# Kernel optimization log

Hardware: AMD Instinct MI355X
Metric: run time of the kernel (lower is better)

Reference implementation:

```python
import jax, jax.numpy as jnp
import numpy as np
from jax import lax

P = 8; E = 192; D_MODEL = E + 4; D_STATE = 16; D_CONV = 4; EXPAND = 2
D_INNER = EXPAND * D_MODEL  # 392
DT_RANK = -(-D_MODEL // 16)  # 13
MAX_FREQ = 32


def silu(v):
    return v * jax.nn.sigmoid(v)


def layernorm(v, g, b, eps=1e-5):
    m = v.mean(-1, keepdims=True)
    var = v.var(-1, keepdims=True)
    return (v - m) / jnp.sqrt(var + eps) * g + b


def mamba(x, in_w, conv_w, conv_b, xp_w, dt_w, dt_b, A_log, Dp, out_w):
    # Standard mamba_ssm Mamba block. x: (B, L, d_model)
    B, L, _ = x.shape
    xz = x @ in_w.T                      # (B,L,2*d_inner)
    xi, z = jnp.split(xz, 2, axis=-1)
    # depthwise causal conv1d (torch pads d_conv-1 both sides then truncates to L)
    xc = jnp.transpose(xi, (0, 2, 1))    # (B,d_inner,L)
    xc = lax.conv_general_dilated(xc, conv_w[:, None, :], (1,), [(D_CONV - 1, 0)],
                                  dimension_numbers=('NCH', 'OIH', 'NCH'),
                                  feature_group_count=D_INNER)
    xc = silu(jnp.transpose(xc, (0, 2, 1)) + conv_b)  # (B,L,d_inner)
    x_dbl = xc @ xp_w.T                  # (B,L,dt_rank+2*d_state)
    dt = x_dbl[..., :DT_RANK]
    Bm = x_dbl[..., DT_RANK:DT_RANK + D_STATE]
    Cm = x_dbl[..., DT_RANK + D_STATE:]
    delta = jax.nn.softplus(dt @ dt_w.T + dt_b)       # (B,L,d_inner)
    A = -jnp.exp(A_log)                               # (d_inner,d_state)
    deltaA = jnp.exp(delta[..., None] * A)            # (B,L,d_inner,d_state)
    deltaBu = delta[..., None] * Bm[:, :, None, :] * xc[..., None]

    def step(h, inp):
        dA, dBu, c = inp
        h = dA * h + dBu
        return h, jnp.einsum('bdn,bn->bd', h, c)

    h0 = jnp.zeros((B, D_INNER, D_STATE), x.dtype)
    _, ys = lax.scan(step, h0, (deltaA.transpose(1, 0, 2, 3),
                                deltaBu.transpose(1, 0, 2, 3),
                                Cm.transpose(1, 0, 2)))
    y = ys.transpose(1, 0, 2) + Dp * xc
    y = y * silu(z)
    return y @ out_w.T


def _mk_mamba_params(key):
    ks = jax.random.split(key, 6)
    s = 0.05
    return dict(
        in_w=jax.random.normal(ks[0], (2 * D_INNER, D_MODEL)) * s,
        conv_w=jax.random.normal(ks[1], (D_INNER, D_CONV)) * s,
        conv_b=jnp.zeros((D_INNER,)),
        xp_w=jax.random.normal(ks[2], (DT_RANK + 2 * D_STATE, D_INNER)) * s,
        dt_w=jax.random.normal(ks[3], (D_INNER, DT_RANK)) * s,
        dt_b=jax.random.normal(ks[4], (D_INNER,)) * 0.1,
        A_log=jnp.log(jnp.broadcast_to(jnp.arange(1, D_STATE + 1, dtype=jnp.float32), (D_INNER, D_STATE)) + 0.0),
        D=jnp.ones((D_INNER,)),
        out_w=jax.random.normal(ks[5], (D_MODEL, D_INNER)) * s,
    )


def setup_inputs() -> dict:
    key = jax.random.key(0)
    k = jax.random.split(key, 8)
    inp = {
        'x': jax.random.normal(k[0], (16, 3, 256, 256), dtype=jnp.float32),
        'patch_w': jax.random.normal(k[1], (E, 3, P, P)) * 0.05,
        'patch_b': jnp.zeros((E,)),
        'pe_ln_g': jnp.ones((E,)), 'pe_ln_b': jnp.zeros((E,)),
        'blk_ln_g': jnp.ones((D_MODEL,)), 'blk_ln_b': jnp.zeros((D_MODEL,)),
        'cls_w': jax.random.normal(k[2], (1, D_MODEL)) * 0.05,
        'cls_b': jnp.zeros((1,)),
    }
    for pref, kk in (('f_', k[3]), ('b_', k[4])):
        for name, val in _mk_mamba_params(kk).items():
            inp[pref + name] = val
    return inp


def reference(x, patch_w, patch_b, pe_ln_g, pe_ln_b,
              f_in_w, f_conv_w, f_conv_b, f_xp_w, f_dt_w, f_dt_b, f_A_log, f_D, f_out_w,
              b_in_w, b_conv_w, b_conv_b, b_xp_w, b_dt_w, b_dt_b, b_A_log, b_D, b_out_w,
              blk_ln_g, blk_ln_b, cls_w, cls_b):
    B, C, H, W = x.shape
    hp, wp = H // P, W // P
    # PatchEmbed: stride==kernel conv expressed as one GEMM over patches
    xp = x.reshape(B, C, hp, P, wp, P)
    tok = jnp.einsum('bchpwq,ecpq->bhwe', xp, patch_w) + patch_b
    tok = tok.reshape(B, hp * wp, E)
    tok = silu(layernorm(tok, pe_ln_g, pe_ln_b))
    # RotaryEmbedding: concat 4 positional channels
    L = hp * wp
    scale = 2 * np.pi / MAX_FREQ
    pos = jnp.arange(L, dtype=tok.dtype)[:, None] * scale
    row = (jnp.arange(L) // MAX_FREQ).astype(tok.dtype)[:, None] * scale
    cp = jnp.concatenate([jnp.sin(pos), jnp.cos(pos), jnp.sin(row), jnp.cos(row)], axis=-1)
    h = jnp.concatenate([tok, jnp.broadcast_to(cp[None], (B, L, 4))], axis=-1)  # (B,L,196)
    # BidirectionalMambaBlock
    fo = mamba(h, f_in_w, f_conv_w, f_conv_b, f_xp_w, f_dt_w, f_dt_b, f_A_log, f_D, f_out_w)
    bo = jnp.flip(mamba(jnp.flip(h, 1), b_in_w, b_conv_w, b_conv_b, b_xp_w, b_dt_w, b_dt_b, b_A_log, b_D, b_out_w), 1)
    out = (fo + bo) * 0.5
    out = silu(layernorm(out, blk_ln_g, blk_ln_b)) + h
    # Classifier: mean pool + linear (num_classes==2 -> 1 logit)
    return out.mean(1) @ cls_w.T + cls_b
```

## Files before the change

### kernel.cpp

```cpp
#include <hip/hip_runtime.h>
#include <cstdint>
#include <cstddef>

constexpr int B_   = 16;
constexpr int L_   = 1024;
constexpr int E_   = 192;
constexpr int DM   = 196;
constexpr int DI   = 392;
constexpr int DS   = 16;
constexpr int DTR  = 13;
constexpr int NTOK = B_ * L_;
constexpr int XDW  = DTR + 2 * DS;
constexpr int CH   = B_ * DI;

constexpr int KP_XZ = 224;
constexpr int KP_OP = 416;
constexpr int KP_PW = 192;

constexpr size_t HW_SZ = (size_t)NTOK * DM;
constexpr size_t DI_SZ = (size_t)NTOK * DI;

constexpr size_t O_H     = 0;
constexpr size_t O_H16   = 3211264;
constexpr size_t O_XI_F  = 5046272;
constexpr size_t O_XI_B  = 11468800;
constexpr size_t O_Z_F   = 17891328;
constexpr size_t O_Z_B   = 24313856;
constexpr size_t O_XC_F  = 30736384;
constexpr size_t O_XC_B  = 37158912;
constexpr size_t O_DTR_F = 43581440;
constexpr size_t O_DTR_B = 43794432;
constexpr size_t O_BC_F  = 44007424;
constexpr size_t O_BC_B  = 44531712;
constexpr size_t O_YS_F  = 45056000;
constexpr size_t O_YS_B  = 48267264;
constexpr size_t O_PW16  = 51478528;
constexpr size_t O_FIN16 = 51496960;
constexpr size_t O_BIN16 = 51584768;
constexpr size_t O_FOUT16= 51672576;
constexpr size_t O_BOUT16= 51713344;

typedef _Float16 half8 __attribute__((ext_vector_type(8)));
typedef _Float16 half4v __attribute__((ext_vector_type(4)));
typedef float f32x4v __attribute__((ext_vector_type(4)));

__device__ __forceinline__ float siluf(float x) {
    return x / (1.f + __expf(-x));
}

__device__ __forceinline__ float blk_sum(float v, float* red) {
    #pragma unroll
    for (int o = 32; o > 0; o >>= 1) v += __shfl_down(v, o);
    int w = threadIdx.x >> 6;
    __syncthreads();
    if ((threadIdx.x & 63) == 0) red[w] = v;
    __syncthreads();
    return red[0] + red[1] + red[2] + red[3];
}

__global__ __launch_bounds__(256) void cvt_all(const float* __restrict__ pw,
                                               const float* __restrict__ fin,
                                               const float* __restrict__ bin,
                                               const float* __restrict__ fout,
                                               const float* __restrict__ bout,
                                               _Float16* __restrict__ dst) {
    int i = blockIdx.x * 256 + threadIdx.x;
    const float* src; int K, Kp, off;
    if (i < 36864)       { src = pw;   K = 192; Kp = 192; off = i; }
    else if (i < 212480) { src = fin;  K = 196; Kp = 224; off = i - 36864; }
    else if (i < 388096) { src = bin;  K = 196; Kp = 224; off = i - 212480; }
    else if (i < 469632) { src = fout; K = 392; Kp = 416; off = i - 388096; }
    else                 { src = bout; K = 392; Kp = 416; off = i - 469632; }
    int n = off / Kp, k = off - n * Kp;
    dst[i] = (_Float16)(k < K ? src[(size_t)n * K + k] : 0.f);
}

__global__ __launch_bounds__(256) void gather_patch(const float* __restrict__ x,
                                                    _Float16* __restrict__ Xp) {
    int i = blockIdx.x * 256 + threadIdx.x;
    int tok = i / 192, r = i - tok * 192;
    int c = r >> 6, pq = r & 63, p = pq >> 3, q = pq & 7;
    int b = tok >> 10, l = tok & 1023, hh = l >> 5, wv = l & 31;
    Xp[i] = (_Float16)x[(((size_t)(b * 3 + c) * 256 + hh * 8 + p) << 8) + wv * 8 + q];
}

template <int MODE>
__device__ __forceinline__ void mfma_core(const _Float16* __restrict__ A,
                                          const _Float16* __restrict__ W,
                                          const float* __restrict__ bias,
                                          void* __restrict__ Cv_,
                                          int N, int Kpad, int ldc,
                                          int flip, int m_blk, int n_blk) {
    const int tid = threadIdx.x;
    const int wv = tid >> 6, lane = tid & 63;
    const int col = lane & 15, quad = lane >> 4;
    const int m_base = m_blk * 128 + wv * 32;
    const int n_base = n_blk * 64;

    int r0 = m_base + col, r1 = m_base + 16 + col;
    if (flip) {
        r0 = (r0 & ~1023) + (1023 - (r0 & 1023));
        r1 = (r1 & ~1023) + (1023 - (r1 & 1023));
    }
    const _Float16* a0p = A + (size_t)r0 * Kpad + quad * 8;
    const _Float16* a1p = A + (size_t)r1 * Kpad + quad * 8;

    const _Float16* bp[4];
    bool bok[4];
    #pragma unroll
    for (int j = 0; j < 4; ++j) {
        int n = n_base + j * 16 + col;
        bok[j] = (n < N);
        bp[j] = W + (size_t)(bok[j] ? n : 0) * Kpad + quad * 8;
    }

    f32x4v acc[2][4];
    #pragma unroll
    for (int i = 0; i < 2; ++i)
        #pragma unroll
        for (int j = 0; j < 4; ++j)
            #pragma unroll
            for (int r = 0; r < 4; ++r) acc[i][j][r] = 0.f;

    half8 bzero;
    #pragma unroll
    for (int q = 0; q < 8; ++q) bzero[q] = (_Float16)0.f;

    for (int k0 = 0; k0 < Kpad; k0 += 32) {
        half8 a0 = *(const half8*)(a0p + k0);
        half8 a1 = *(const half8*)(a1p + k0);
        #pragma unroll
        for (int j = 0; j < 4; ++j) {
            half8 bv = bzero;
            if (bok[j]) bv = *(const half8*)(bp[j] + k0);
            acc[0][j] = __builtin_amdgcn_mfma_f32_16x16x32_f16(a0, bv, acc[0][j], 0, 0, 0);
            acc[1][j] = __builtin_amdgcn_mfma_f32_16x16x32_f16(a1, bv, acc[1][j], 0, 0, 0);
        }
    }

    if (MODE == 0) {
        float* C = (float*)Cv_;
        #pragma unroll
        for (int i = 0; i < 2; ++i) {
            int mrow = m_base + i * 16 + quad * 4;
            #pragma unroll
            for (int j = 0; j < 4; ++j) {
                int n = n_base + j * 16 + col;
                if (n < N) {
                    float bv = bias ? bias[n] : 0.f;
                    #pragma unroll
                    for (int r = 0; r < 4; ++r)
                        C[(size_t)(mrow + r) * ldc + n] = acc[i][j][r] + bv;
                }
            }
        }
    } else if (MODE == 4) {
        _Float16* C = (_Float16*)Cv_;
        #pragma unroll
        for (int i = 0; i < 2; ++i) {
            int mrow = m_base + i * 16 + quad * 4;
            #pragma unroll
            for (int j = 0; j < 4; ++j) {
                int n = n_base + j * 16 + col;
                if (n < N) {
                    #pragma unroll
                    for (int r = 0; r < 4; ++r)
                        C[(size_t)(mrow + r) * ldc + n] = (_Float16)acc[i][j][r];
                }
            }
        }
    } else {
        const int bb = m_base >> 10;
        const int t0 = m_base & 1023;
        #pragma unroll
        for (int i = 0; i < 2; ++i) {
            int tt = t0 + i * 16 + quad * 4;
            #pragma unroll
            for (int j = 0; j < 4; ++j) {
                int n = n_base + j * 16 + col;
                if (n < N) {
                    half4v v;
                    #pragma unroll
                    for (int r = 0; r < 4; ++r) {
                        float xx = acc[i][j][r];
                        if (MODE == 3) xx = xx / (1.f + __expf(-xx));
                        v[r] = (_Float16)xx;
                    }
                    *(half4v*)((_Float16*)Cv_ + (((size_t)(bb * N + n)) << 10) + tt) = v;
                }
            }
        }
    }
}

__global__ __launch_bounds__(256) void mfma_patch(const _Float16* __restrict__ A,
                                                  const _Float16* __restrict__ W,
                                                  const float* __restrict__ bias,
                                                  float* __restrict__ C) {
    mfma_core<0>(A, W, bias, C, 192, KP_PW, 192, 0, blockIdx.x, blockIdx.y);
}

__global__ __launch_bounds__(256) void mfma_xz(const _Float16* __restrict__ A,
                                               const _Float16* __restrict__ Wf,
                                               const _Float16* __restrict__ Wb,
                                               _Float16* __restrict__ C0, _Float16* __restrict__ C1,
                                               _Float16* __restrict__ C2, _Float16* __restrict__ C3) {
    const int zi = blockIdx.z;
    const _Float16* W = (zi < 2 ? Wf : Wb) + (size_t)(zi & 1) * DI * KP_XZ;
    const int flip = zi >> 1;
    if (zi == 0)      mfma_core<2>(A, W, nullptr, C0, DI, KP_XZ, 0, flip, blockIdx.x, blockIdx.y);
    else if (zi == 1) mfma_core<3>(A, W, nullptr, C1, DI, KP_XZ, 0, flip, blockIdx.x, blockIdx.y);
    else if (zi == 2) mfma_core<2>(A, W, nullptr, C2, DI, KP_XZ, 0, flip, blockIdx.x, blockIdx.y);
    else              mfma_core<3>(A, W, nullptr, C3, DI, KP_XZ, 0, flip, blockIdx.x, blockIdx.y);
}

__global__ __launch_bounds__(256) void mfma_op(const _Float16* __restrict__ Af,
                                               const _Float16* __restrict__ Ab,
                                               const _Float16* __restrict__ Wf,
                                               const _Float16* __restrict__ Wb,
                                               _Float16* __restrict__ Cf, _Float16* __restrict__ Cb) {
    const int zi = blockIdx.z;
    mfma_core<4>(zi ? Ab : Af, zi ? Wb : Wf, nullptr, zi ? Cb : Cf,
                 DM, KP_OP, DM, 0, blockIdx.x, blockIdx.y);
}

__global__ __launch_bounds__(256) void ln_silu_pos(const float* __restrict__ tok,
                                                   const float* __restrict__ g,
                                                   const float* __restrict__ bb,
                                                   _Float16* __restrict__ h16) {
    const int w = threadIdx.x >> 6, lane = threadIdx.x & 63;
    const int t = blockIdx.x * 4 + w;
    const float* tp = tok + (size_t)t * E_;
    float v[3];
    float s1 = 0.f, s2 = 0.f;
    #pragma unroll
    for (int i = 0; i < 3; ++i) {
        v[i] = tp[lane + i * 64];
        s1 += v[i];
        s2 = fmaf(v[i], v[i], s2);
    }
    #pragma unroll
    for (int o = 32; o > 0; o >>= 1) {
        s1 += __shfl_xor(s1, o);
        s2 += __shfl_xor(s2, o);
    }
    float mean = s1 * (1.f / E_);
    float var = s2 * (1.f / E_) - mean * mean;
    float inv = rsqrtf(var + 1e-5f);
    _Float16* hq = h16 + (size_t)t * KP_XZ;
    #pragma unroll
    for (int i = 0; i < 3; ++i) {
        int e = lane + i * 64;
        float o = siluf((v[i] - mean) * inv * g[e] + bb[e]);
        hq[e] = (_Float16)o;
    }
    const int l = t & 1023;
    const float scale = 0.19634954084936207f;
    if (lane < 4) {
        float pv = (lane == 0) ? sinf(l * scale)
                 : (lane == 1) ? cosf(l * scale)
                 : (lane == 2) ? sinf((float)(l >> 5) * scale)
                 :               cosf((float)(l >> 5) * scale);
        hq[E_ + lane] = (_Float16)pv;
    } else if (lane < 32) {
        hq[192 + lane] = (_Float16)0.f;
    }
}

__global__ __launch_bounds__(256) void gemm_xdbl(const _Float16* __restrict__ xi_f,
                                                 const _Float16* __restrict__ xi_b,
                                                 const float* __restrict__ Wf,
                                                 const float* __restrict__ Wb,
                                                 const float* __restrict__ fcw,
                                                 const float* __restrict__ fcb,
                                                 const float* __restrict__ bcw,
                                                 const float* __restrict__ bcb,
                                                 float* __restrict__ dtrf,
                                                 float* __restrict__ dtrb,
                                                 float* __restrict__ bcf,
                                                 float* __restrict__ bcb2,
                                                 float* __restrict__ xcf,
                                                 float* __restrict__ xcb) {
    const int yi = blockIdx.y;
    const _Float16* xi = yi ? xi_b : xi_f;
    const float* W = yi ? Wb : Wf;
    const float* cw = yi ? bcw : fcw;
    const float* cb = yi ? bcb : fcb;
    float* dtr = yi ? dtrb : dtrf;
    float* bc = yi ? bcb2 : bcf;
    float* xc = yi ? xcb : xcf;
    __shared__ __align__(16) float As[16][68];
    __shared__ __align__(16) float Ws[16][68];
    const int m0 = blockIdx.x * 64;
    const int t = threadIdx.x;
    const int tx = t & 15, ty = t >> 4;
    float acc[4][4] = {};
    const int arow_l = t >> 2;
    const int kq = (t & 3) * 4;
    const int bb_ = m0 >> 10, tt0 = m0 & 1023;
    for (int kt = 0; kt < 25; ++kt) {
        const int k0 = kt << 4;
        {
            int kr = t >> 4, tc = t & 15;
            int kk = k0 + kr;
            float o4[4] = {0.f, 0.f, 0.f, 0.f};
            if (kk < DI) {
                const int tpos = tt0 + tc * 4;
                const _Float16* xp = xi + (((size_t)(bb_ * DI + kk)) << 10) + tpos;
                half4v cur = *(const half4v*)xp;
                half4v prv;
                if (tpos > 0) prv = *(const half4v*)(xp - 4);
                else { prv[0] = prv[1] = prv[2] = prv[3] = (_Float16)0.f; }
                float xw[7] = {(float)prv[1], (float)prv[2], (float)prv[3],
                               (float)cur[0], (float)cur[1], (float)cur[2], (float)cur[3]};
                float4 wv4 = *(const float4*)(cw + kk * 4);
                float wc[4] = {wv4.x, wv4.y, wv4.z, wv4.w};
                float bv = cb[kk];
                #pragma unroll
                for (int j = 0; j < 4; ++j) {
                    float a = bv;
                    #pragma unroll
                    for (int q = 0; q < 4; ++q) a = fmaf(xw[j + q], wc[q], a);
                    o4[j] = siluf(a);
                }
                *(float4*)(xc + (((size_t)(bb_ * DI + kk)) << 10) + tpos) =
                    *(float4*)o4;
            }
            *(float4*)&As[kr][tc * 4] = *(float4*)o4;
        }
        {
            bool okn = arow_l < XDW;
            const float* wp = W + (size_t)arow_l * DI;
            #pragma unroll
            for (int jj = 0; jj < 4; ++jj) {
                int kk = k0 + kq + jj;
                Ws[kq + jj][arow_l] = (okn && kk < DI) ? wp[kk] : 0.f;
            }
        }
        __syncthreads();
        #pragma unroll
        for (int k = 0; k < 16; ++k) {
            float av[4], wv[4];
            *(float4*)av = *(const float4*)&As[k][ty * 4];
            *(float4*)wv = *(const float4*)&Ws[k][tx * 4];
            #pragma unroll
            for (int i = 0; i < 4; ++i)
                #pragma unroll
                for (int j = 0; j < 4; ++j)
                    acc[i][j] = fmaf(av[i], wv[j], acc[i][j]);
        }
        __syncthreads();
    }
    #pragma unroll
    for (int i = 0; i < 4; ++i) {
        int m = m0 + ty * 4 + i;
        #pragma unroll
        for (int j = 0; j < 4; ++j) {
            int n = tx * 4 + j;
            float v = acc[i][j];
            if (n < DTR) dtr[(size_t)m * DTR + n] = v;
            else if (n < XDW) bc[(size_t)m * 32 + (n - DTR)] = v;
        }
    }
}

__global__ __launch_bounds__(256) void delta_kernel(
        const float* __restrict__ dtr_f, const float* __restrict__ dtr_b,
        float* __restrict__ dlT_f, float* __restrict__ dlT_b,
        const float* __restrict__ f_dt_w, const float* __restrict__ f_dt_b,
        const float* __restrict__ b_dt_w, const float* __restrict__ b_dt_b) {
    int i = blockIdx.x * 256 + threadIdx.x;
    int dir = i >= (int)DI_SZ;
    int j = dir ? i - (int)DI_SZ : i;
    int r = j >> 10, t = j & 1023;
    int b = r / DI, d = r - (r / DI) * DI;
    size_t tok = ((size_t)b << 10) + t;
    const float* xd = (dir ? dtr_b : dtr_f) + tok * DTR;
    const float* w = (dir ? b_dt_w : f_dt_w) + d * DTR;
    float acc = (dir ? b_dt_b : f_dt_b)[d];
    #pragma unroll
    for (int q = 0; q < DTR; ++q) acc = fmaf(xd[q], w[q], acc);
    float sp = fmaxf(acc, 0.f) + log1pf(__expf(-fabsf(acc)));
    (dir ? dlT_b : dlT_f)[j] = sp;
}

__global__ __launch_bounds__(256) void scan_kernel(
        const float* __restrict__ dlT_f, const float* __restrict__ dlT_b,
        const float* __restrict__ xcT_f, const float* __restrict__ xcT_b,
        const float* __restrict__ bc_f,  const float* __restrict__ bc_b,
        const _Float16* __restrict__ zT_f, const _Float16* __restrict__ zT_b,
        _Float16* __restrict__ y16_f,    _Float16* __restrict__ y16_b,
        const float* __restrict__ fA, const float* __restrict__ bA,
        const float* __restrict__ fD, const float* __restrict__ bD) {
    __shared__ float sP[8][8][16];
    __shared__ float sH[8][8][16];
    __shared__ float sI[8][8][16];
    const int tid = threadIdx.x;
    const int ni = tid & 3;
    const int c  = (tid >> 2) & 7;
    const int ch_l = tid >> 5;
    const int chain = blockIdx.x * 8 + ch_l;
    const int dir = chain >= CH;
    const int r = chain - (dir ? CH : 0);
    const int b = r / DI, d = r - (r / DI) * DI;

    const float* dlT = (dir ? dlT_b : dlT_f) + ((size_t)r << 10);
    const float* uT  = (dir ? xcT_b : xcT_f) + ((size_t)r << 10);
    const _Float16* zT = (dir ? zT_b : zT_f) + ((size_t)r << 10);
    const float* BC  = (dir ? bc_b  : bc_f)  + (((size_t)b << 10) * 32);
    _Float16* y16    = (dir ? y16_b : y16_f) + ((size_t)r << 10);
    const float* Al  = (dir ? bA : fA) + d * DS + ni * 4;
    float Av[4];
    #pragma unroll
    for (int i = 0; i < 4; ++i) Av[i] = -__expf(Al[i]) * 1.4426950408889634f;
    const float Dd = (dir ? bD : fD)[d];
    const int t0 = c << 7;

    if (c < 7) {
        float h[4] = {0.f, 0.f, 0.f, 0.f};
        float S = 0.f;
        for (int g = 0; g < 32; ++g) {
            const int tg = t0 + g * 4;
            float4 d4 = *(const float4*)(dlT + tg);
            float4 u4 = *(const float4*)(uT + tg);
            float dv[4] = {d4.x, d4.y, d4.z, d4.w};
            float uv[4] = {u4.x, u4.y, u4.z, u4.w};
            #pragma unroll
            for (int tt = 0; tt < 4; ++tt) {
                float4 B4 = *(const float4*)(BC + (size_t)(tg + tt) * 32 + ni * 4);
                float w = dv[tt] * uv[tt];
                S += dv[tt];
                float Bv[4] = {B4.x, B4.y, B4.z, B4.w};
                #pragma unroll
                for (int i = 0; i < 4; ++i)
                    h[i] = fmaf(exp2f(dv[tt] * Av[i]), h[i], w * Bv[i]);
            }
        }
        #pragma unroll
        for (int i = 0; i < 4; ++i) {
            sP[ch_l][c][ni * 4 + i] = exp2f(S * Av[i]);
            sH[ch_l][c][ni * 4 + i] = h[i];
        }
    }
    __syncthreads();

    if (tid < 128) {
        const int ch = tid >> 4, n = tid & 15;
        float hi = 0.f;
        #pragma unroll
        for (int cc = 0; cc < 8; ++cc) {
            sI[ch][cc][n] = hi;
            if (cc < 7) hi = sH[ch][cc][n] + sP[ch][cc][n] * hi;
        }
    }
    __syncthreads();

    {
        float h[4];
        #pragma unroll
        for (int i = 0; i < 4; ++i) h[i] = sI[ch_l][c][ni * 4 + i];
        _Float16 ybuf[8] __attribute__((aligned(16)));
        half8 zb;
        for (int g = 0; g < 32; ++g) {
            if ((g & 7) == 0)
                zb = *(const half8*)(zT + t0 + ((g >> 3) << 5) + ni * 8);
            const int tg = t0 + g * 4;
            float4 d4 = *(const float4*)(dlT + tg);
            float4 u4 = *(const float4*)(uT + tg);
            float dv[4] = {d4.x, d4.y, d4.z, d4.w};
            float uv[4] = {u4.x, u4.y, u4.z, u4.w};
            float pq[4];
            #pragma unroll
            for (int tt = 0; tt < 4; ++tt) {
                float4 B4 = *(const float4*)(BC + (size_t)(tg + tt) * 32 + ni * 4);
                float4 C4 = *(const float4*)(BC + (size_t)(tg + tt) * 32 + 16 + ni * 4);
                float w = dv[tt] * uv[tt];
                float Bv[4] = {B4.x, B4.y, B4.z, B4.w};
                float Cv[4] = {C4.x, C4.y, C4.z, C4.w};
                float p = 0.f;
                #pragma unroll
                for (int i = 0; i < 4; ++i) {
                    h[i] = fmaf(exp2f(dv[tt] * Av[i]), h[i], w * Bv[i]);
                    p = fmaf(h[i], Cv[i], p);
                }
                pq[tt] = p;
            }
            #pragma unroll
            for (int tt = 0; tt < 4; ++tt) {
                pq[tt] += __shfl_xor(pq[tt], 1);
                pq[tt] += __shfl_xor(pq[tt], 2);
            }
            if (((g >> 1) & 3) == ni) {
                const int base = (g & 1) * 4;
                #pragma unroll
                for (int tt = 0; tt < 4; ++tt)
                    ybuf[base + tt] =
                        (_Float16)((pq[tt] + Dd * uv[tt]) * (float)zb[base + tt]);
            }
            if ((g & 7) == 7)
                *(half8*)(y16 + t0 + ((g >> 3) << 5) + ni * 8) = *(half8*)ybuf;
        }
    }
}

__global__ __launch_bounds__(256) void transp_y(
        const _Float16* __restrict__ yf, const _Float16* __restrict__ yb,
        _Float16* __restrict__ of, _Float16* __restrict__ ob) {
    __shared__ _Float16 tile[64][72];
    const int dblk = blockIdx.z % 7, dir = blockIdx.z / 7;
    const int b = blockIdx.y, tb = blockIdx.x;
    const _Float16* y = dir ? yb : yf;
    _Float16* o = dir ? ob : of;
    const int d0 = dblk * 64, t0 = tb * 64;
    const int dl = threadIdx.x >> 2, ts = (threadIdx.x & 3) * 16;
    const int d = d0 + dl;
    if (d < DI) {
        const _Float16* src = y + (((size_t)(b * DI + d)) << 10) + t0 + ts;
        *(half8*)&tile[dl][ts] = *(const half8*)src;
        *(half8*)&tile[dl][ts + 8] = *(const half8*)(src + 8);
    } else {
        #pragma unroll
        for (int q = 0; q < 16; ++q) tile[dl][ts + q] = (_Float16)0.f;
    }
    __syncthreads();
    const int tl = threadIdx.x >> 2, ds = (threadIdx.x & 3) * 16;
    if (d0 + ds < KP_OP) {
        _Float16 v[16] __attribute__((aligned(16)));
        #pragma unroll
        for (int q = 0; q < 16; ++q) v[q] = tile[ds + q][tl];
        _Float16* dst = o + ((size_t)((b << 10) + t0 + tl)) * KP_OP + d0 + ds;
        *(half8*)dst = *(half8*)&v[0];
        *(half8*)(dst + 8) = *(half8*)&v[8];
    }
}

__global__ __launch_bounds__(256) void final_head(
        const _Float16* __restrict__ fo, const _Float16* __restrict__ bo,
        const _Float16* __restrict__ h16, const float* __restrict__ g,
        const float* __restrict__ bb, const float* __restrict__ cls_w,
        float* __restrict__ partial) {
    const int w = threadIdx.x >> 6, lane = threadIdx.x & 63;
    const int t = blockIdx.x * 4 + w;
    const int b = t >> 10, l = t & 1023;
    const _Float16* fp = fo + (size_t)t * DM;
    const _Float16* bp = bo + ((size_t)(b << 10) + (1023 - l)) * DM;
    const _Float16* hp = h16 + (size_t)t * KP_XZ;
    float v[4];
    float s1 = 0.f, s2 = 0.f;
    #pragma unroll
    for (int i = 0; i < 4; ++i) {
        int e = lane + i * 64;
        bool ok = (i < 3) || (lane < 4);
        float vv = ok ? 0.5f * ((float)fp[e] + (float)bp[e]) : 0.f;
        v[i] = vv;
        s1 += vv;
        s2 = fmaf(vv, vv, s2);
    }
    #pragma unroll
    for (int o = 32; o > 0; o >>= 1) {
        s1 += __shfl_xor(s1, o);
        s2 += __shfl_xor(s2, o);
    }
    float mean = s1 * (1.f / DM);
    float var = s2 * (1.f / DM) - mean * mean;
    float inv = rsqrtf(var + 1e-5f);
    float c = 0.f;
    #pragma unroll
    for (int i = 0; i < 4; ++i) {
        int e = lane + i * 64;
        bool ok = (i < 3) || (lane < 4);
        if (ok) {
            float o2 = (v[i] - mean) * inv * g[e] + bb[e];
            o2 = siluf(o2) + (float)hp[e];
            c = fmaf(o2, cls_w[e], c);
        }
    }
    #pragma unroll
    for (int o = 32; o > 0; o >>= 1) c += __shfl_xor(c, o);
    if (lane == 0) partial[t] = c;
}

__global__ __launch_bounds__(256) void head_reduce(const float* __restrict__ partial,
                                                   const float* __restrict__ cls_b,
                                                   float* __restrict__ out) {
    __shared__ float red[4];
    const int b = blockIdx.x;
    const float* p = partial + ((size_t)b << 10);
    float s = 0.f;
    for (int i = threadIdx.x; i < 1024; i += 256) s += p[i];
    s = blk_sum(s, red);
    if (threadIdx.x == 0) out[b] = s * (1.f / 1024.f) + cls_b[0];
}

extern "C" void kernel_launch(void* const* d_in, const int* in_sizes, int n_in,
                              void* d_out, int out_size, void* d_ws, size_t ws_size,
                              hipStream_t stream) {
    const float* x        = (const float*)d_in[0];
    const float* patch_w  = (const float*)d_in[1];
    const float* patch_b  = (const float*)d_in[2];
    const float* pe_g     = (const float*)d_in[3];
    const float* pe_b     = (const float*)d_in[4];
    const float* blk_g    = (const float*)d_in[5];
    const float* blk_b    = (const float*)d_in[6];
    const float* cls_w    = (const float*)d_in[7];
    const float* cls_b    = (const float*)d_in[8];
    const float* f_in_w   = (const float*)d_in[9];
    const float* f_conv_w = (const float*)d_in[10];
    const float* f_conv_b = (const float*)d_in[11];
    const float* f_xp_w   = (const float*)d_in[12];
    const float* f_dt_w   = (const float*)d_in[13];
    const float* f_dt_b   = (const float*)d_in[14];
    const float* f_A_log  = (const float*)d_in[15];
    const float* f_D      = (const float*)d_in[16];
    const float* f_out_w  = (const float*)d_in[17];
    const float* b_in_w   = (const float*)d_in[18];
    const float* b_conv_w = (const float*)d_in[19];
    const float* b_conv_b = (const float*)d_in[20];
    const float* b_xp_w   = (const float*)d_in[21];
    const float* b_dt_w   = (const float*)d_in[22];
    const float* b_dt_b   = (const float*)d_in[23];
    const float* b_A_log  = (const float*)d_in[24];
    const float* b_D      = (const float*)d_in[25];
    const float* b_out_w  = (const float*)d_in[26];

    float* ws = (float*)d_ws;
    float* out = (float*)d_out;

    _Float16* H16    = (_Float16*)(ws + O_H16);
    _Float16* XI16f  = (_Float16*)(ws + O_XI_F);
    _Float16* XI16b  = (_Float16*)(ws + O_XI_B);
    float* DLf       = ws + O_XI_F;
    float* DLb       = ws + O_XI_B;
    _Float16* FO16   = (_Float16*)(ws + O_XI_F);
    _Float16* BO16   = (_Float16*)(ws + O_XI_B);
    _Float16* ZT16f  = (_Float16*)(ws + O_Z_F);
    _Float16* ZT16b  = (_Float16*)(ws + O_Z_B);
    _Float16* YsTf16 = (_Float16*)(ws + O_Z_F);
    _Float16* YsTb16 = (_Float16*)(ws + O_Z_B);
    float* XCf       = ws + O_XC_F;
    float* XCb       = ws + O_XC_B;
    float* DTRf      = ws + O_DTR_F;
    float* DTRb      = ws + O_DTR_B;
    float* BCf       = ws + O_BC_F;
    float* BCb       = ws + O_BC_B;
    _Float16* Xp16   = (_Float16*)(ws + O_YS_F);
    float* TokRaw    = ws + O_YS_B;
    _Float16* Y16f   = (_Float16*)(ws + O_YS_F);
    _Float16* Y16b   = (_Float16*)(ws + O_YS_B);
    _Float16* PW16   = (_Float16*)(ws + O_PW16);
    _Float16* FIN16  = (_Float16*)(ws + O_FIN16);
    _Float16* BIN16  = (_Float16*)(ws + O_BIN16);
    _Float16* FOUT16 = (_Float16*)(ws + O_FOUT16);
    _Float16* BOUT16 = (_Float16*)(ws + O_BOUT16);

    cvt_all<<<2153, 256, 0, stream>>>(patch_w, f_in_w, b_in_w, f_out_w, b_out_w, PW16);

    gather_patch<<<(NTOK * 192) / 256, 256, 0, stream>>>(x, Xp16);
    mfma_patch<<<dim3(NTOK / 128, 3), 256, 0, stream>>>(Xp16, PW16, patch_b, TokRaw);
    ln_silu_pos<<<NTOK / 4, 256, 0, stream>>>(TokRaw, pe_g, pe_b, H16);

    mfma_xz<<<dim3(NTOK / 128, 7, 4), 256, 0, stream>>>(H16, FIN16, BIN16,
                                                        XI16f, ZT16f, XI16b, ZT16b);
    gemm_xdbl<<<dim3(NTOK / 64, 2), 256, 0, stream>>>(
        XI16f, XI16b, f_xp_w, b_xp_w, f_conv_w, f_conv_b, b_conv_w, b_conv_b,
        DTRf, DTRb, BCf, BCb, XCf, XCb);
    delta_kernel<<<(2 * (int)DI_SZ) / 256, 256, 0, stream>>>(
        DTRf, DTRb, DLf, DLb, f_dt_w, f_dt_b, b_dt_w, b_dt_b);
    scan_kernel<<<2 * CH / 8, 256, 0, stream>>>(
        DLf, DLb, XCf, XCb, BCf, BCb, ZT16f, ZT16b, Y16f, Y16b,
        f_A_log, b_A_log, f_D, b_D);
    transp_y<<<dim3(16, 16, 14), 256, 0, stream>>>(Y16f, Y16b, YsTf16, YsTb16);
    mfma_op<<<dim3(NTOK / 128, 4, 2), 256, 0, stream>>>(YsTf16, YsTb16,
                                                        FOUT16, BOUT16, FO16, BO16);
    final_head<<<NTOK / 4, 256, 0, stream>>>(FO16, BO16, H16, blk_g, blk_b, cls_w, XCf);
    head_reduce<<<B_, 256, 0, stream>>>(XCf, cls_b, out);
}
```

Before: 503.0 us.

## Vectorize patch gather, stage MFMA epilogues through LDS, use raw exp2 in scan

```diff
diff --git a/kernel.cpp b/kernel.cpp
--- a/kernel.cpp
+++ b/kernel.cpp
@@ -47,6 +47,9 @@
 __device__ __forceinline__ float siluf(float x) {
     return x / (1.f + __expf(-x));
 }
+__device__ __forceinline__ float fexp2(float x) {
+    return __builtin_amdgcn_exp2f(x);
+}
 
 __device__ __forceinline__ float blk_sum(float v, float* red) {
     #pragma unroll
@@ -78,10 +81,16 @@
 __global__ __launch_bounds__(256) void gather_patch(const float* __restrict__ x,
                                                     _Float16* __restrict__ Xp) {
     int i = blockIdx.x * 256 + threadIdx.x;
-    int tok = i / 192, r = i - tok * 192;
-    int c = r >> 6, pq = r & 63, p = pq >> 3, q = pq & 7;
+    int tok = i / 24, r = i - tok * 24;
+    int c = r >> 3, p = r & 7;
     int b = tok >> 10, l = tok & 1023, hh = l >> 5, wv = l & 31;
-    Xp[i] = (_Float16)x[(((size_t)(b * 3 + c) * 256 + hh * 8 + p) << 8) + wv * 8 + q];
+    const float* src = x + (((size_t)(b * 3 + c) * 256 + hh * 8 + p) << 8) + wv * 8;
+    float4 v0 = *(const float4*)src;
+    float4 v1 = *(const float4*)(src + 4);
+    half8 o;
+    o[0] = (_Float16)v0.x; o[1] = (_Float16)v0.y; o[2] = (_Float16)v0.z; o[3] = (_Float16)v0.w;
+    o[4] = (_Float16)v1.x; o[5] = (_Float16)v1.y; o[6] = (_Float16)v1.z; o[7] = (_Float16)v1.w;
+    *(half8*)(Xp + (size_t)tok * 192 + c * 64 + p * 8) = o;
 }
 
 template <int MODE>
@@ -138,7 +147,7 @@
         }
     }
 
-    if (MODE == 0) {
+    if constexpr (MODE == 0) {
         float* C = (float*)Cv_;
         #pragma unroll
         for (int i = 0; i < 2; ++i) {
@@ -154,40 +163,65 @@
                 }
             }
         }
-    } else if (MODE == 4) {
+    } else if constexpr (MODE == 2 || MODE == 3) {
+        __shared__ _Float16 cst[64 * 136];
+        #pragma unroll
+        for (int i = 0; i < 2; ++i) {
+            int t_loc = wv * 32 + i * 16 + quad * 4;
+            #pragma unroll
+            for (int j = 0; j < 4; ++j) {
+                int n_loc = j * 16 + col;
+                half4v v;
+                #pragma unroll
+                for (int r = 0; r < 4; ++r) {
+                    float xx = acc[i][j][r];
+                    if (MODE == 3) xx = xx / (1.f + __expf(-xx));
+                    v[r] = (_Float16)xx;
+                }
+                *(half4v*)&cst[n_loc * 136 + t_loc] = v;
+            }
+        }
+        __syncthreads();
+        const int n_loc = tid >> 2, chunk = tid & 3;
+        const int n = n_base + n_loc;
+        if (n < N) {
+            const int bb = (m_blk * 128) >> 10;
+            const int t0b = (m_blk * 128) & 1023;
+            _Float16* dst = (_Float16*)Cv_ + (((size_t)(bb * N + n)) << 10) + t0b + chunk * 32;
+            const _Float16* s = &cst[n_loc * 136 + chunk * 32];
+            #pragma unroll
+            for (int q = 0; q < 4; ++q)
+                *(half8*)(dst + q * 8) = *(const half8*)(s + q * 8);
+        }
+    } else {
+        __shared__ _Float16 cst[128 * 72];
+        #pragma unroll
+        for (int i = 0; i < 2; ++i) {
+            #pragma unroll
+            for (int j = 0; j < 4; ++j) {
+                int n_loc = j * 16 + col;
+                #pragma unroll
+                for (int r = 0; r < 4; ++r) {
+                    int m_loc = wv * 32 + i * 16 + quad * 4 + r;
+                    cst[m_loc * 72 + n_loc] = (_Float16)acc[i][j][r];
+                }
+            }
+        }
+        __syncthreads();
+        const int m_loc = tid >> 1, half = tid & 1;
+        const int m = m_blk * 128 + m_loc;
         _Float16* C = (_Float16*)Cv_;
-        #pragma unroll
-        for (int i = 0; i < 2; ++i) {
-            int mrow = m_base + i * 16 + quad * 4;
-            #pragma unroll
-            for (int j = 0; j < 4; ++j) {
-                int n = n_base + j * 16 + col;
-                if (n < N) {
-                    #pragma unroll
-                    for (int r = 0; r < 4; ++r)
-                        C[(size_t)(mrow + r) * ldc + n] = (_Float16)acc[i][j][r];
-                }
-            }
-        }
-    } else {
-        const int bb = m_base >> 10;
-        const int t0 = m_base & 1023;
-        #pragma unroll
-        for (int i = 0; i < 2; ++i) {
-            int tt = t0 + i * 16 + quad * 4;
-            #pragma unroll
-            for (int j = 0; j < 4; ++j) {
-                int n = n_base + j * 16 + col;
-                if (n < N) {
-                    half4v v;
-                    #pragma unroll
-                    for (int r = 0; r < 4; ++r) {
-                        float xx = acc[i][j][r];
-                        if (MODE == 3) xx = xx / (1.f + __expf(-xx));
-                        v[r] = (_Float16)xx;
-                    }
-                    *(half4v*)((_Float16*)Cv_ + (((size_t)(bb * N + n)) << 10) + tt) = v;
-                }
+        const _Float16* s = &cst[m_loc * 72 + half * 32];
+        if (n_base + 64 <= N) {
+            _Float16* dst = C + (size_t)m * ldc + n_base + half * 32;
+            #pragma unroll
+            for (int q = 0; q < 4; ++q)
+                *(half8*)(dst + q * 8) = *(const half8*)(s + q * 8);
+        } else {
+            #pragma unroll
+            for (int q = 0; q < 32; ++q) {
+                int n = n_base + half * 32 + q;
+                if (n < N) C[(size_t)m * ldc + n] = s[q];
             }
         }
     }
@@ -419,26 +453,29 @@
     if (c < 7) {
         float h[4] = {0.f, 0.f, 0.f, 0.f};
         float S = 0.f;
+        const float* bcp = BC + t0 * 32 + ni * 4;
+        const float* dp = dlT + t0;
+        const float* up = uT + t0;
         for (int g = 0; g < 32; ++g) {
-            const int tg = t0 + g * 4;
-            float4 d4 = *(const float4*)(dlT + tg);
-            float4 u4 = *(const float4*)(uT + tg);
+            float4 d4 = *(const float4*)(dp + g * 4);
+            float4 u4 = *(const float4*)(up + g * 4);
             float dv[4] = {d4.x, d4.y, d4.z, d4.w};
             float uv[4] = {u4.x, u4.y, u4.z, u4.w};
             #pragma unroll
             for (int tt = 0; tt < 4; ++tt) {
-                float4 B4 = *(const float4*)(BC + (size_t)(tg + tt) * 32 + ni * 4);
+                float4 B4 = *(const float4*)(bcp + tt * 32);
                 float w = dv[tt] * uv[tt];
                 S += dv[tt];
                 float Bv[4] = {B4.x, B4.y, B4.z, B4.w};
                 #pragma unroll
                 for (int i = 0; i < 4; ++i)
-                    h[i] = fmaf(exp2f(dv[tt] * Av[i]), h[i], w * Bv[i]);
-            }
+                    h[i] = fmaf(fexp2(dv[tt] * Av[i]), h[i], w * Bv[i]);
+            }
+            bcp += 128;
         }
         #pragma unroll
         for (int i = 0; i < 4; ++i) {
-            sP[ch_l][c][ni * 4 + i] = exp2f(S * Av[i]);
+            sP[ch_l][c][ni * 4 + i] = fexp2(S * Av[i]);
             sH[ch_l][c][ni * 4 + i] = h[i];
         }
     }
@@ -461,30 +498,33 @@
         for (int i = 0; i < 4; ++i) h[i] = sI[ch_l][c][ni * 4 + i];
         _Float16 ybuf[8] __attribute__((aligned(16)));
         half8 zb;
+        const float* bcp = BC + t0 * 32 + ni * 4;
+        const float* dp = dlT + t0;
+        const float* up = uT + t0;
         for (int g = 0; g < 32; ++g) {
             if ((g & 7) == 0)
                 zb = *(const half8*)(zT + t0 + ((g >> 3) << 5) + ni * 8);
-            const int tg = t0 + g * 4;
-            float4 d4 = *(const float4*)(dlT + tg);
-            float4 u4 = *(const float4*)(uT + tg);
+            float4 d4 = *(const float4*)(dp + g * 4);
+            float4 u4 = *(const float4*)(up + g * 4);
             float dv[4] = {d4.x, d4.y, d4.z, d4.w};
             float uv[4] = {u4.x, u4.y, u4.z, u4.w};
             float pq[4];
             #pragma unroll
             for (int tt = 0; tt < 4; ++tt) {
-                float4 B4 = *(const float4*)(BC + (size_t)(tg + tt) * 32 + ni * 4);
-                float4 C4 = *(const float4*)(BC + (size_t)(tg + tt) * 32 + 16 + ni * 4);
+                float4 B4 = *(const float4*)(bcp + tt * 32);
+                float4 C4 = *(const float4*)(bcp + tt * 32 + 16);
                 float w = dv[tt] * uv[tt];
                 float Bv[4] = {B4.x, B4.y, B4.z, B4.w};
                 float Cv[4] = {C4.x, C4.y, C4.z, C4.w};
                 float p = 0.f;
                 #pragma unroll
                 for (int i = 0; i < 4; ++i) {
-                    h[i] = fmaf(exp2f(dv[tt] * Av[i]), h[i], w * Bv[i]);
+                    h[i] = fmaf(fexp2(dv[tt] * Av[i]), h[i], w * Bv[i]);
                     p = fmaf(h[i], Cv[i], p);
                 }
                 pq[tt] = p;
             }
+            bcp += 128;
             #pragma unroll
             for (int tt = 0; tt < 4; ++tt) {
                 pq[tt] += __shfl_xor(pq[tt], 1);
@@ -655,7 +695,7 @@
 
     cvt_all<<<2153, 256, 0, stream>>>(patch_w, f_in_w, b_in_w, f_out_w, b_out_w, PW16);
 
-    gather_patch<<<(NTOK * 192) / 256, 256, 0, stream>>>(x, Xp16);
+    gather_patch<<<(NTOK * 24) / 256, 256, 0, stream>>>(x, Xp16);
     mfma_patch<<<dim3(NTOK / 128, 3), 256, 0, stream>>>(Xp16, PW16, patch_b, TokRaw);
     ln_silu_pos<<<NTOK / 4, 256, 0, stream>>>(TokRaw, pe_g, pe_b, H16);
 
```

New measurement: 473.3 us. 1.06x faster.
